# Kernel tuning notes

Measured on AMD Instinct MI355X. Metric: run time of the kernel, lower is better.

## Reference

```python
import jax, jax.numpy as jnp
import numpy as np

NEG_INF = -9e15
ALPHA = 2.0  # LeakyReLU negative slope from init (alpha=2)


def setup_inputs() -> dict:
    key = jax.random.key(0)
    k1, k2, k3, k4 = jax.random.split(key, 4)
    B, N, Fin, Fout = 8, 2048, 256, 128
    x = jax.random.normal(k1, (B, N, Fin), dtype=jnp.float32)
    adj = jax.random.randint(k2, (B, N, N), 0, 2, dtype=jnp.int32)
    # xavier_uniform with gain=1.414
    def xavier(k, shape, gain=1.414):
        fan_in, fan_out = shape[0], shape[1]
        bound = gain * np.sqrt(6.0 / (fan_in + fan_out))
        return jax.random.uniform(k, shape, jnp.float32, -bound, bound)
    W = xavier(k3, (Fin, Fout))
    a = xavier(k4, (2 * Fout, 1))
    return {"x": x, "adj": adj, "W": W, "a": a}


def reference(x, adj, W, a):
    # Wh: [B, N, Fout]
    Wh = jnp.matmul(x, W)
    Fout = W.shape[1]
    a1 = a[:Fout, 0]   # [Fout]
    a2 = a[Fout:, 0]   # [Fout]
    f1 = jnp.einsum('bnf,f->bn', Wh, a1)  # [B, N]
    f2 = jnp.einsum('bnf,f->bn', Wh, a2)  # [B, N]
    e = f1[:, :, None] + f2[:, None, :]   # [B, N, N]
    e = jnp.where(e >= 0, e, ALPHA * e)   # leaky relu, slope 2
    e = jnp.where(adj > 0, e, NEG_INF)
    attention = jax.nn.softmax(e, axis=2)
    # dropout: eval mode (no-op)
    h_prime = jnp.matmul(attention, Wh)   # [B, N, Fout]
    # concat=True -> elu
    return jnp.where(h_prime > 0, h_prime, jnp.expm1(h_prime))
```

## Files before the change

### kernel.cpp

```cpp
#include <hip/hip_runtime.h>
#include <hip/hip_bf16.h>
#include <math.h>

#define NEGINF (-9000000000000000.0f)

constexpr int B_   = 8;
constexpr int N_   = 2048;
constexpr int FIN  = 256;
constexpr int FOUT = 128;

constexpr int CH  = 512;
constexpr int NCH = N_ / CH;
constexpr int PR  = CH + 8;
constexpr int XR  = FIN + 8;

typedef __attribute__((ext_vector_type(8))) short bf16x8;
typedef __attribute__((ext_vector_type(4))) float f32x4;

static __device__ __forceinline__ unsigned short f2bf(float f) {
    __hip_bfloat16 h = __float2bfloat16(f);
    return *reinterpret_cast<unsigned short*>(&h);
}

__global__ __launch_bounds__(256) void k0_wt(const float* __restrict__ W,
                                             unsigned short* __restrict__ Wt) {
    const int n = blockIdx.x;
    const int k = threadIdx.x;
    Wt[n * FIN + k] = f2bf(W[k * FOUT + n]);
}

__global__ __launch_bounds__(256) void ka_wh(const float* __restrict__ x,
                                             const unsigned short* __restrict__ Wt,
                                             const float* __restrict__ a,
                                             unsigned short* __restrict__ WhT,
                                             float* __restrict__ f1,
                                             float* __restrict__ f2) {
    __shared__ unsigned short xs[32 * XR];
    __shared__ float as[2 * FOUT];
    __shared__ float fred[2][4][32];

    const int tid = threadIdx.x;
    const int j0  = blockIdx.x * 32;
    const int b   = j0 >> 11;
    const int jb  = j0 & (N_ - 1);

    if (tid < 2 * FOUT) as[tid] = a[tid];
    {
        const float4* xsrc = (const float4*)(x + (size_t)j0 * FIN);
#pragma unroll
        for (int t = 0; t < 8; ++t) {
            const int idx = tid + t * 256;
            float4 v = xsrc[idx];
            const int row = idx >> 6, c4 = idx & 63;
            ushort4 u;
            u.x = f2bf(v.x); u.y = f2bf(v.y); u.z = f2bf(v.z); u.w = f2bf(v.w);
            *(ushort4*)&xs[row * XR + c4 * 4] = u;
        }
    }
    __syncthreads();

    const int wave = tid >> 6, lane = tid & 63;
    const int quad = lane >> 4, l16 = lane & 15;

    f32x4 acc[2][2];
#pragma unroll
    for (int aa = 0; aa < 2; ++aa)
#pragma unroll
        for (int nn = 0; nn < 2; ++nn) acc[aa][nn] = {0.f, 0.f, 0.f, 0.f};

    const unsigned short* wtA0 = Wt + (size_t)(32 * wave + l16) * FIN;
    const unsigned short* wtA1 = wtA0 + 16 * FIN;
#pragma unroll
    for (int ks = 0; ks < FIN / 32; ++ks) {
        const int kof = ks * 32 + quad * 8;
        bf16x8 af0 = *(const bf16x8*)&wtA0[kof];
        bf16x8 af1 = *(const bf16x8*)&wtA1[kof];
        bf16x8 bf0 = *(const bf16x8*)&xs[l16 * XR + kof];
        bf16x8 bf1 = *(const bf16x8*)&xs[(16 + l16) * XR + kof];
        acc[0][0] = __builtin_amdgcn_mfma_f32_16x16x32_bf16(af0, bf0, acc[0][0], 0, 0, 0);
        acc[0][1] = __builtin_amdgcn_mfma_f32_16x16x32_bf16(af0, bf1, acc[0][1], 0, 0, 0);
        acc[1][0] = __builtin_amdgcn_mfma_f32_16x16x32_bf16(af1, bf0, acc[1][0], 0, 0, 0);
        acc[1][1] = __builtin_amdgcn_mfma_f32_16x16x32_bf16(af1, bf1, acc[1][1], 0, 0, 0);
    }

    unsigned short* dst = WhT + (size_t)b * FOUT * N_;
    float pf[2][2] = {{0.f, 0.f}, {0.f, 0.f}};
#pragma unroll
    for (int aa = 0; aa < 2; ++aa)
#pragma unroll
        for (int nn = 0; nn < 2; ++nn)
#pragma unroll
            for (int r = 0; r < 4; ++r) {
                const int d = 32 * wave + 16 * aa + 4 * quad + r;
                const int j = jb + 16 * nn + l16;
                const float v = acc[aa][nn][r];
                dst[(size_t)d * N_ + j] = f2bf(v);
                pf[0][nn] += v * as[d];
                pf[1][nn] += v * as[FOUT + d];
            }
#pragma unroll
    for (int ff = 0; ff < 2; ++ff)
#pragma unroll
        for (int nn = 0; nn < 2; ++nn) {
            float v = pf[ff][nn];
            v += __shfl_xor(v, 16);
            v += __shfl_xor(v, 32);
            pf[ff][nn] = v;
        }
    if (quad == 0) {
#pragma unroll
        for (int ff = 0; ff < 2; ++ff)
#pragma unroll
            for (int nn = 0; nn < 2; ++nn)
                fred[ff][wave][nn * 16 + l16] = pf[ff][nn];
    }
    __syncthreads();
    if (tid < 64) {
        const int ff = tid >> 5, j32 = tid & 31;
        const float s = fred[ff][0][j32] + fred[ff][1][j32] +
                        fred[ff][2][j32] + fred[ff][3][j32];
        (ff ? f2 : f1)[(size_t)b * N_ + jb + j32] = s;
    }
}

__global__ __launch_bounds__(256) void kb_attn(const int* __restrict__ adj,
                                               const unsigned short* __restrict__ WhT,
                                               const float* __restrict__ f1,
                                               const float* __restrict__ f2,
                                               float* __restrict__ out) {
    __shared__ unsigned short p[16 * PR];
    __shared__ float alpha_s[16];
    __shared__ float rsum[16];

    const int tid  = threadIdx.x;
    const int b    = blockIdx.x & 7;
    const int i0   = (blockIdx.x >> 3) * 16;
    const int wave = tid >> 6, lane = tid & 63;
    const int quad = lane >> 4, l16 = lane & 15;

    const float4* f2b4 = (const float4*)(f2 + (size_t)b * N_);

    float m_run[4], s_run[4];
#pragma unroll
    for (int r = 0; r < 4; ++r) { m_run[r] = NEGINF; s_run[r] = 0.f; }

    f32x4 acc0 = {0.f, 0.f, 0.f, 0.f}, acc1 = {0.f, 0.f, 0.f, 0.f};
    const int n0 = wave * 32;
    const unsigned short* wB0 = WhT + (size_t)b * FOUT * N_ + (size_t)(n0 + l16) * N_;
    const unsigned short* wB1 = wB0 + (size_t)16 * N_;
    const unsigned short* pA  = &p[l16 * PR];

    for (int c = 0; c < NCH; ++c) {
#pragma unroll
        for (int rr = 0; rr < 4; ++rr) {
            const int ti = wave * 4 + rr;
            const int i  = i0 + ti;
            const float f1i = f1[(size_t)b * N_ + i];
            const int4* arow4 = (const int4*)(adj + ((size_t)b * N_ + i) * (size_t)N_);
            const int c4 = c * (CH / 4);
            int4   av0 = arow4[c4 + lane];
            int4   av1 = arow4[c4 + 64 + lane];
            float4 fv0 = f2b4[c4 + lane];
            float4 fv1 = f2b4[c4 + 64 + lane];

            float e[8];
            e[0] = f1i + fv0.x; e[1] = f1i + fv0.y; e[2] = f1i + fv0.z; e[3] = f1i + fv0.w;
            e[4] = f1i + fv1.x; e[5] = f1i + fv1.y; e[6] = f1i + fv1.z; e[7] = f1i + fv1.w;
#pragma unroll
            for (int q = 0; q < 8; ++q) e[q] = (e[q] >= 0.f) ? e[q] : 2.f * e[q];
            if (av0.x <= 0) e[0] = NEGINF;
            if (av0.y <= 0) e[1] = NEGINF;
            if (av0.z <= 0) e[2] = NEGINF;
            if (av0.w <= 0) e[3] = NEGINF;
            if (av1.x <= 0) e[4] = NEGINF;
            if (av1.y <= 0) e[5] = NEGINF;
            if (av1.z <= 0) e[6] = NEGINF;
            if (av1.w <= 0) e[7] = NEGINF;

            float mx = e[0];
#pragma unroll
            for (int q = 1; q < 8; ++q) mx = fmaxf(mx, e[q]);
#pragma unroll
            for (int o = 32; o; o >>= 1) mx = fmaxf(mx, __shfl_xor(mx, o));

            const float mnew = fmaxf(m_run[rr], mx);
            const float al   = __expf(m_run[rr] - mnew);
            float pv[8];
            float s8 = 0.f;
#pragma unroll
            for (int q = 0; q < 8; ++q) { pv[q] = __expf(e[q] - mnew); s8 += pv[q]; }
#pragma unroll
            for (int o = 32; o; o >>= 1) s8 += __shfl_xor(s8, o);
            s_run[rr] = s_run[rr] * al + s8;
            m_run[rr] = mnew;

            ushort4 u0, u1;
            u0.x = f2bf(pv[0]); u0.y = f2bf(pv[1]); u0.z = f2bf(pv[2]); u0.w = f2bf(pv[3]);
            u1.x = f2bf(pv[4]); u1.y = f2bf(pv[5]); u1.z = f2bf(pv[6]); u1.w = f2bf(pv[7]);
            *(ushort4*)&p[ti * PR + 4 * lane]       = u0;
            *(ushort4*)&p[ti * PR + 256 + 4 * lane] = u1;
            if (lane == 0) alpha_s[ti] = al;
            if (c == NCH - 1 && lane == 0) rsum[ti] = s_run[rr];
        }
        __syncthreads();

#pragma unroll
        for (int r = 0; r < 4; ++r) {
            const float alr = alpha_s[quad * 4 + r];
            acc0[r] *= alr;
            acc1[r] *= alr;
        }
        const int kbase = c * CH;
#pragma unroll
        for (int ks = 0; ks < CH / 32; ++ks) {
            const int kof = ks * 32 + quad * 8;
            bf16x8 afr = *(const bf16x8*)&pA[kof];
            bf16x8 b0  = *(const bf16x8*)&wB0[kbase + kof];
            bf16x8 b1  = *(const bf16x8*)&wB1[kbase + kof];
            acc0 = __builtin_amdgcn_mfma_f32_16x16x32_bf16(afr, b0, acc0, 0, 0, 0);
            acc1 = __builtin_amdgcn_mfma_f32_16x16x32_bf16(afr, b1, acc1, 0, 0, 0);
        }
        __syncthreads();
    }

#pragma unroll
    for (int r = 0; r < 4; ++r) {
        const int m = quad * 4 + r;
        const float inv = 1.f / rsum[m];
        float v0 = acc0[r] * inv;
        float v1 = acc1[r] * inv;
        v0 = (v0 > 0.f) ? v0 : expm1f(v0);
        v1 = (v1 > 0.f) ? v1 : expm1f(v1);
        const size_t base = ((size_t)b * N_ + i0 + m) * FOUT + n0;
        out[base + l16]      = v0;
        out[base + 16 + l16] = v1;
    }
}

extern "C" void kernel_launch(void* const* d_in, const int* in_sizes, int n_in,
                              void* d_out, int out_size, void* d_ws, size_t ws_size,
                              hipStream_t stream) {
    const float* x   = (const float*)d_in[0];
    const int*   adj = (const int*)d_in[1];
    const float* W   = (const float*)d_in[2];
    const float* a   = (const float*)d_in[3];
    float* out = (float*)d_out;

    unsigned short* WhT = (unsigned short*)d_ws;
    unsigned short* Wt  = WhT + (size_t)B_ * FOUT * N_;
    float* f1 = (float*)(Wt + (size_t)FOUT * FIN);
    float* f2 = f1 + (size_t)B_ * N_;

    hipLaunchKernelGGL(k0_wt, dim3(FOUT), dim3(FIN), 0, stream, W, Wt);
    hipLaunchKernelGGL(ka_wh, dim3(B_ * N_ / 32), dim3(256), 0, stream,
                       x, Wt, a, WhT, f1, f2);
    hipLaunchKernelGGL(kb_attn, dim3(B_ * N_ / 16), dim3(256), 0, stream,
                       adj, WhT, f1, f2, out);
}
```

Measured before the change: 266.6 us.

## Pack adjacency into bitmask and stage WhT stores through LDS

Adds a pre-pass kernel that streams the int32 adjacency matrix once and packs it into a 1-bit-per-entry mask with wave ballots. The attention kernel then reads 4 mask bits per lane instead of eight int32 loads. This takes the large, latency-heavy adjacency reads out of the compute-heavy softmax/MFMA loop. The projection kernel now writes its transposed bf16 output through shared memory, so the global stores become 16-byte coalesced vectors, and the f1 loads are hoisted out of the chunk loop. The trade-off is an extra kernel launch plus a small mask write and read, while the full adjacency still has to be read once.

```diff
diff --git a/kernel.cpp b/kernel.cpp
--- a/kernel.cpp
+++ b/kernel.cpp
@@ -13,6 +13,7 @@
 constexpr int NCH = N_ / CH;
 constexpr int PR  = CH + 8;
 constexpr int XR  = FIN + 8;
+constexpr int TR  = 40;
 
 typedef __attribute__((ext_vector_type(8))) short bf16x8;
 typedef __attribute__((ext_vector_type(4))) float f32x4;
@@ -27,6 +28,26 @@
     const int n = blockIdx.x;
     const int k = threadIdx.x;
     Wt[n * FIN + k] = f2bf(W[k * FOUT + n]);
+}
+
+__global__ __launch_bounds__(256) void kadj(const int* __restrict__ adj,
+                                            unsigned long long* __restrict__ mask) {
+    const int tid  = threadIdx.x;
+    const int wave = tid >> 6, lane = tid & 63;
+    const size_t row = (size_t)blockIdx.x * 4 + wave;
+    const int* src = adj + row * N_;
+    unsigned long long* dst = mask + row * (N_ / 64);
+#pragma unroll
+    for (int g = 0; g < 4; ++g) {
+        unsigned long long m[8];
+#pragma unroll
+        for (int q = 0; q < 8; ++q)
+            m[q] = __ballot(src[g * 512 + q * 64 + lane] > 0);
+        unsigned long long v = m[0];
+#pragma unroll
+        for (int q = 1; q < 8; ++q) v = (lane == q) ? m[q] : v;
+        if (lane < 8) dst[g * 8 + lane] = v;
+    }
 }
 
 __global__ __launch_bounds__(256) void ka_wh(const float* __restrict__ x,
@@ -82,8 +103,9 @@
         acc[1][0] = __builtin_amdgcn_mfma_f32_16x16x32_bf16(af1, bf0, acc[1][0], 0, 0, 0);
         acc[1][1] = __builtin_amdgcn_mfma_f32_16x16x32_bf16(af1, bf1, acc[1][1], 0, 0, 0);
     }
-
-    unsigned short* dst = WhT + (size_t)b * FOUT * N_;
+    __syncthreads();
+
+    unsigned short* T = xs;
     float pf[2][2] = {{0.f, 0.f}, {0.f, 0.f}};
 #pragma unroll
     for (int aa = 0; aa < 2; ++aa)
@@ -92,9 +114,8 @@
 #pragma unroll
             for (int r = 0; r < 4; ++r) {
                 const int d = 32 * wave + 16 * aa + 4 * quad + r;
-                const int j = jb + 16 * nn + l16;
                 const float v = acc[aa][nn][r];
-                dst[(size_t)d * N_ + j] = f2bf(v);
+                T[d * TR + nn * 16 + l16] = f2bf(v);
                 pf[0][nn] += v * as[d];
                 pf[1][nn] += v * as[FOUT + d];
             }
@@ -115,6 +136,15 @@
                 fred[ff][wave][nn * 16 + l16] = pf[ff][nn];
     }
     __syncthreads();
+
+    unsigned short* dstW = WhT + (size_t)b * FOUT * N_;
+#pragma unroll
+    for (int it = 0; it < 2; ++it) {
+        const int idx = it * 256 + tid;
+        const int d = idx >> 2, q = idx & 3;
+        bf16x8 v = *(const bf16x8*)&T[d * TR + q * 8];
+        *(bf16x8*)&dstW[(size_t)d * N_ + jb + q * 8] = v;
+    }
     if (tid < 64) {
         const int ff = tid >> 5, j32 = tid & 31;
         const float s = fred[ff][0][j32] + fred[ff][1][j32] +
@@ -123,7 +153,7 @@
     }
 }
 
-__global__ __launch_bounds__(256) void kb_attn(const int* __restrict__ adj,
+__global__ __launch_bounds__(256) void kb_attn(const unsigned int* __restrict__ mask32,
                                                const unsigned short* __restrict__ WhT,
                                                const float* __restrict__ f1,
                                                const float* __restrict__ f2,
@@ -140,9 +170,13 @@
 
     const float4* f2b4 = (const float4*)(f2 + (size_t)b * N_);
 
-    float m_run[4], s_run[4];
-#pragma unroll
-    for (int r = 0; r < 4; ++r) { m_run[r] = NEGINF; s_run[r] = 0.f; }
+    float f1r[4], m_run[4], s_run[4];
+#pragma unroll
+    for (int rr = 0; rr < 4; ++rr) {
+        f1r[rr]   = f1[(size_t)b * N_ + i0 + wave * 4 + rr];
+        m_run[rr] = NEGINF;
+        s_run[rr] = 0.f;
+    }
 
     f32x4 acc0 = {0.f, 0.f, 0.f, 0.f}, acc1 = {0.f, 0.f, 0.f, 0.f};
     const int n0 = wave * 32;
@@ -155,11 +189,14 @@
         for (int rr = 0; rr < 4; ++rr) {
             const int ti = wave * 4 + rr;
             const int i  = i0 + ti;
-            const float f1i = f1[(size_t)b * N_ + i];
-            const int4* arow4 = (const int4*)(adj + ((size_t)b * N_ + i) * (size_t)N_);
+            const float f1i = f1r[rr];
+            const unsigned int* mrow =
+                mask32 + ((size_t)b * N_ + i) * (N_ / 32);
+            const unsigned int w0 = mrow[c * 16 + (lane >> 3)];
+            const unsigned int w1 = mrow[c * 16 + 8 + (lane >> 3)];
+            const unsigned int t0 = (w0 >> ((lane & 7) * 4)) & 0xF;
+            const unsigned int t1 = (w1 >> ((lane & 7) * 4)) & 0xF;
             const int c4 = c * (CH / 4);
-            int4   av0 = arow4[c4 + lane];
-            int4   av1 = arow4[c4 + 64 + lane];
             float4 fv0 = f2b4[c4 + lane];
             float4 fv1 = f2b4[c4 + 64 + lane];
 
@@ -168,14 +205,11 @@
             e[4] = f1i + fv1.x; e[5] = f1i + fv1.y; e[6] = f1i + fv1.z; e[7] = f1i + fv1.w;
 #pragma unroll
             for (int q = 0; q < 8; ++q) e[q] = (e[q] >= 0.f) ? e[q] : 2.f * e[q];
-            if (av0.x <= 0) e[0] = NEGINF;
-            if (av0.y <= 0) e[1] = NEGINF;
-            if (av0.z <= 0) e[2] = NEGINF;
-            if (av0.w <= 0) e[3] = NEGINF;
-            if (av1.x <= 0) e[4] = NEGINF;
-            if (av1.y <= 0) e[5] = NEGINF;
-            if (av1.z <= 0) e[6] = NEGINF;
-            if (av1.w <= 0) e[7] = NEGINF;
+#pragma unroll
+            for (int q = 0; q < 4; ++q) {
+                if (!((t0 >> q) & 1)) e[q]     = NEGINF;
+                if (!((t1 >> q) & 1)) e[4 + q] = NEGINF;
+            }
 
             float mx = e[0];
 #pragma unroll
@@ -250,10 +284,12 @@
     unsigned short* Wt  = WhT + (size_t)B_ * FOUT * N_;
     float* f1 = (float*)(Wt + (size_t)FOUT * FIN);
     float* f2 = f1 + (size_t)B_ * N_;
-
+    unsigned long long* mask = (unsigned long long*)(f2 + (size_t)B_ * N_);
+
+    hipLaunchKernelGGL(kadj, dim3(B_ * N_ / 4), dim3(256), 0, stream, adj, mask);
     hipLaunchKernelGGL(k0_wt, dim3(FOUT), dim3(FIN), 0, stream, W, Wt);
     hipLaunchKernelGGL(ka_wh, dim3(B_ * N_ / 32), dim3(256), 0, stream,
                        x, Wt, a, WhT, f1, f2);
     hipLaunchKernelGGL(kb_attn, dim3(B_ * N_ / 16), dim3(256), 0, stream,
-                       adj, WhT, f1, f2, out);
-}
+                       (const unsigned int*)mask, WhT, f1, f2, out);
+}
```

Result: slower. 285.7 us (+7.2%).
